# Optimization experiments

Hardware: AMD Instinct MI355X
Metric: run time of the kernel (lower is better)

## Reference

```python
import jax, jax.numpy as jnp
import numpy as np

N = 50000      # num nodes
C_IN = 128     # channels[0]
C_OUT = 128    # channels[1]
D = 16         # fixed node degree
T = 4          # diffusion steps
H_MLP = 64     # diff_mlp hidden
H_GRU = 128    # GRUAggr hidden
EPS = 0.01


def setup_inputs() -> dict:
    key = jax.random.key(0)
    ks = jax.random.split(key, 10)
    node_attr = jax.random.normal(ks[0], (N, C_IN), jnp.float32)
    # adjacency sorted by source: node i owns columns [i*D, i*D+D)
    src = jnp.repeat(jnp.arange(N), D)
    dst = jax.random.randint(ks[1], (N * D,), 0, N)
    edge_index = jnp.stack([src, dst])                       # [2, N*D]
    slices = jnp.stack([jnp.arange(N) * D, jnp.full((N,), D)], axis=1)  # [N,2] (start,count)
    noise = EPS * jax.random.normal(ks[2], (T, N, D), jnp.float32)      # eps*randn per step
    init = lambda k, shape, fan: (jax.random.normal(k, shape, jnp.float32) / np.sqrt(fan))
    W1 = init(ks[3], ((1 + T) * C_IN, H_MLP), (1 + T) * C_IN)
    b1 = jnp.zeros((H_MLP,), jnp.float32)
    W2 = init(ks[4], (H_MLP, 1), H_MLP)
    b2 = jnp.zeros((1,), jnp.float32)
    Wx = init(ks[5], (C_IN, 3 * H_GRU), C_IN)
    Wh = init(ks[6], (H_GRU, 3 * H_GRU), H_GRU)
    bx = jnp.zeros((3 * H_GRU,), jnp.float32)
    bh = jnp.zeros((3 * H_GRU,), jnp.float32)
    Wo = init(ks[7], (H_GRU, C_OUT), H_GRU)
    bo = jnp.zeros((C_OUT,), jnp.float32)
    return dict(node_attr=node_attr, edge_index=edge_index, slices=slices, noise=noise,
                W1=W1, b1=b1, W2=W2, b2=b2, Wx=Wx, Wh=Wh, bx=bx, bh=bh, Wo=Wo, bo=bo)


def _gru(x_seq, Wx, Wh, bx, bh):
    # x_seq: [T+1, N, C]; torch GRU gate order (r, z, n)
    H = Wh.shape[0]
    def step(h, x):
        gx = x @ Wx + bx
        gh = h @ Wh + bh
        xr, xz, xn = jnp.split(gx, 3, axis=-1)
        hr, hz, hn = jnp.split(gh, 3, axis=-1)
        r = jax.nn.sigmoid(xr + hr)
        z = jax.nn.sigmoid(xz + hz)
        n = jnp.tanh(xn + r * hn)
        return (1.0 - z) * n + z * h, None
    h0 = jnp.zeros((x_seq.shape[1], H), x_seq.dtype)
    h, _ = jax.lax.scan(step, h0, x_seq)
    return h


def reference(node_attr, edge_index, slices, noise, W1, b1, W2, b2, Wx, Wh, bx, bh, Wo, bo):
    n, C = node_attr.shape
    t_steps, _, deg = noise.shape
    dst = edge_index[1]
    walk_embeds = jnp.zeros((n, 1 + t_steps, C), node_attr.dtype).at[:, 0, :].set(node_attr)
    cur = jnp.arange(n)
    for t in range(t_steps):
        starts = slices[cur, 0]                              # slice_cat(adj, adj_slic_t)
        nbr = dst[starts[:, None] + jnp.arange(deg)]         # [N, D] neighbor node ids
        v_t = node_attr[nbr]                                 # [N, D, C]
        # diff_mlp on [prefix walk embed | candidate neighbor]: split the first
        # linear layer so the shared prefix is computed once per node (position
        # 1+t of walk_embeds is still zero, matching the original fill order).
        h_pre = walk_embeds.reshape(n, (1 + t_steps) * C) @ W1 + b1       # [N, H_MLP]
        h_nbr = jnp.einsum('ndc,ch->ndh', v_t, W1[(1 + t) * C:(2 + t) * C])
        logp = (jax.nn.relu(h_pre[:, None, :] + h_nbr) @ W2)[..., 0] + b2[0]  # [N, D]
        logp = jax.lax.stop_gradient(logp)                   # torch.no_grad()
        # scatter_logsumexp over init node == logsumexp over the D candidates
        p = jnp.exp(logp - jax.nn.logsumexp(logp, axis=1, keepdims=True)) + noise[t]
        sel = jnp.argmax(p, axis=1)                          # scatter_max per init node
        cur = nbr[jnp.arange(n), sel]                        # walks_t
        walk_embeds = walk_embeds.at[:, 1 + t, :].set(node_attr[cur])
    h = _gru(jnp.transpose(walk_embeds, (1, 0, 2)), Wx, Wh, bx, bh)
    return h @ Wo + bo                                       # [N, C_OUT]
```

## Files before the change

### kernel.cpp

```cpp
#include <hip/hip_runtime.h>
#include <math.h>

#define NND 50000
#define DEG 16

typedef __attribute__((ext_vector_type(8))) short short8v;
typedef __attribute__((ext_vector_type(4))) float float4v;

#define OFF_HPRE 0ULL
#define OFF_PROJ 12800000ULL
#define OFF_XB   64000000ULL
#define OFF_IDX  102400000ULL
#define OFF_BQF  103600384ULL
#define OFF_WOF  103862528ULL
#define WS_NEED  103895296ULL

#define LOG2E 1.44269504088896f

__device__ __forceinline__ float fast_sig(float x){
    return __builtin_amdgcn_rcpf(1.f + __builtin_amdgcn_exp2f(-LOG2E*x));
}
__device__ __forceinline__ float fast_tanh(float x){
    return fmaf(-2.f, __builtin_amdgcn_rcpf(1.f + __builtin_amdgcn_exp2f((2.f*LOG2E)*x)), 1.f);
}
__device__ __forceinline__ unsigned short f2bf(float f){
    unsigned int u = __float_as_uint(f);
    u += 0x7FFFu + ((u >> 16) & 1u);
    return (unsigned short)(u >> 16);
}
__device__ __forceinline__ float bf2f(unsigned short h){
    return __uint_as_float(((unsigned int)h) << 16);
}

__global__ __launch_bounds__(256) void k_iota(int* __restrict__ idx0){
    int i = blockIdx.x*256 + threadIdx.x;
    if (i < NND) idx0[i] = i;
}

__global__ __launch_bounds__(256) void k_projall(const float* __restrict__ A,
    const float* __restrict__ W1, const float* __restrict__ b1,
    float* __restrict__ hpre, float* __restrict__ proj)
{
    __shared__ float Alt[32][320];
    __shared__ float Bl[32][68];
    const int tid = threadIdx.x;
    const int row0 = blockIdx.x << 8;
    const int y = blockIdx.y;
    const float* B = W1 + (size_t)y*128*64;
    const int row_t = tid >> 4, col_t = tid & 15;
    float4 acc[16];
#pragma unroll
    for (int i=0;i<16;i++) acc[i] = make_float4(0.f,0.f,0.f,0.f);

    for (int k0 = 0; k0 < 128; k0 += 32){
        {
            int gr = row0 + tid; if (gr >= NND) gr = NND-1;
            const float* ap = A + (size_t)gr*128 + k0;
            const int sr = tid + ((tid>>4)<<2);
#pragma unroll
            for (int u=0;u<8;u++){
                float4 v = *(const float4*)(ap + (u<<2));
                Alt[(u<<2)+0][sr] = v.x; Alt[(u<<2)+1][sr] = v.y;
                Alt[(u<<2)+2][sr] = v.z; Alt[(u<<2)+3][sr] = v.w;
            }
        }
#pragma unroll
        for (int r=0;r<2;r++){
            int p = (r<<8) + tid;
            int bk = p >> 4, bc = (p & 15) << 2;
            *(float4*)(&Bl[bk][bc]) = *(const float4*)(B + (size_t)(k0+bk)*64 + bc);
        }
        __syncthreads();
#pragma unroll 2
        for (int k=0;k<32;k++){
            const float* ar = &Alt[k][row_t*20];
            float4 a0 = *(const float4*)(ar);
            float4 a1 = *(const float4*)(ar+4);
            float4 a2 = *(const float4*)(ar+8);
            float4 a3 = *(const float4*)(ar+12);
            float4 b  = *(const float4*)(&Bl[k][col_t<<2]);
            float aa[16] = {a0.x,a0.y,a0.z,a0.w, a1.x,a1.y,a1.z,a1.w,
                            a2.x,a2.y,a2.z,a2.w, a3.x,a3.y,a3.z,a3.w};
#pragma unroll
            for (int j=0;j<16;j++){
                acc[j].x = fmaf(aa[j], b.x, acc[j].x);
                acc[j].y = fmaf(aa[j], b.y, acc[j].y);
                acc[j].z = fmaf(aa[j], b.z, acc[j].z);
                acc[j].w = fmaf(aa[j], b.w, acc[j].w);
            }
        }
        __syncthreads();
    }
    float4 bb = make_float4(0.f,0.f,0.f,0.f);
    if (y == 0) bb = *(const float4*)(b1 + (col_t<<2));
    float* dstp = (y == 0) ? hpre : (proj + (size_t)(y-1)*NND*64);
#pragma unroll
    for (int j=0;j<16;j++){
        int gr = row0 + (row_t<<4) + j;
        if (gr < NND){
            float4 o = make_float4(acc[j].x+bb.x, acc[j].y+bb.y, acc[j].z+bb.z, acc[j].w+bb.w);
            *(float4*)(dstp + ((size_t)gr<<6) + (col_t<<2)) = o;
        }
    }
}

__global__ __launch_bounds__(256) void k_walk4(
    const float* __restrict__ hpre0, const float* __restrict__ proj,
    const int* __restrict__ dst, const float* __restrict__ W2,
    const float* __restrict__ b2, const float* __restrict__ noise,
    int* __restrict__ idxb)
{
    const int tid = threadIdx.x;
    const int sg = tid >> 4, l = tid & 15;
    const int gi = (blockIdx.x << 4) + sg;
    float4 hp = *(const float4*)(hpre0 + ((size_t)gi<<6) + (l<<2));
    float4 w2 = *(const float4*)(W2 + (l<<2));
    const float b2s = b2[0];
    int curv = gi;
#pragma unroll 1
    for (int t=0; t<4; t++){
        const float* pj = proj + (size_t)t*NND*64;
        const int nbr = dst[curv*DEG + l];
        float4 val[16];
#pragma unroll
        for (int d=0; d<16; d++){
            int nd = __shfl(nbr, d, 16);
            val[d] = *(const float4*)(pj + ((size_t)nd<<6) + (l<<2));
        }
        float lp = 0.f;
#pragma unroll
        for (int d=0; d<16; d++){
            float4 v = val[d];
            float q =  fmaxf(hp.x+v.x,0.f)*w2.x;
            q = fmaf(fmaxf(hp.y+v.y,0.f), w2.y, q);
            q = fmaf(fmaxf(hp.z+v.z,0.f), w2.z, q);
            q = fmaf(fmaxf(hp.w+v.w,0.f), w2.w, q);
            q += __shfl_xor(q, 1, 16);
            q += __shfl_xor(q, 2, 16);
            q += __shfl_xor(q, 4, 16);
            q += __shfl_xor(q, 8, 16);
            if (l == d) lp = q + b2s;
        }
        float mx = lp;
#pragma unroll
        for (int off=8; off; off>>=1) mx = fmaxf(mx, __shfl_xor(mx, off, 16));
        float s = expf(lp - mx);
#pragma unroll
        for (int off=8; off; off>>=1) s += __shfl_xor(s, off, 16);
        float p = expf(lp - mx - logf(s)) + noise[(size_t)t*NND*DEG + ((size_t)gi<<4) + l];
        float bv = p; int bi = l;
#pragma unroll
        for (int off=8; off; off>>=1){
            float ov = __shfl_xor(bv, off, 16);
            int   oi = __shfl_xor(bi, off, 16);
            if (ov > bv || (ov == bv && oi < bi)){ bv = ov; bi = oi; }
        }
        int sel = __shfl(nbr, bi, 16);
        if (l == 0) idxb[(size_t)(t+1)*NND + gi] = sel;
        float4 u = *(const float4*)(pj + ((size_t)sel<<6) + (l<<2));
        hp.x += u.x; hp.y += u.y; hp.z += u.z; hp.w += u.w;
        curv = sel;
    }
}

__global__ __launch_bounds__(256) void k_pack_x(const float* __restrict__ na,
    unsigned short* __restrict__ Xb)
{
    int i = blockIdx.x*256 + threadIdx.x;
    if (i < NND*32){
        float4 v = *(const float4*)(na + (size_t)i*4);
        unsigned long long pk = (unsigned long long)f2bf(v.x)
            | ((unsigned long long)f2bf(v.y) << 16)
            | ((unsigned long long)f2bf(v.z) << 32)
            | ((unsigned long long)f2bf(v.w) << 48);
        *(unsigned long long*)(Xb + (size_t)i*4) = pk;
    }
}

__global__ __launch_bounds__(256) void k_pack_bqf(const float* __restrict__ Wx,
    const float* __restrict__ Wh, unsigned short* __restrict__ BqF)
{
    int i = blockIdx.x*256 + threadIdx.x;
    int jj = i & 7, lane = (i>>3)&63, ct = (i>>9)&7, c = (i>>12)&7, y = i>>15;
    int g = ct>>1, jh = ct&1, mm = lane&15, quad = lane>>4;
    int jg = (y<<5) + (jh<<4) + mm;
    int k = (c<<5) + (quad<<3) + jj;
    float v = 0.f;
    if (k < 128){
        if (g < 3) v = Wh[k*384 + g*128 + jg];
    } else {
        int kk = k - 128;
        if (g == 0)      v = Wx[kk*384 + jg];
        else if (g == 1) v = Wx[kk*384 + 128 + jg];
        else if (g == 3) v = Wx[kk*384 + 256 + jg];
    }
    BqF[i] = f2bf(v);
}

__global__ __launch_bounds__(256) void k_pack_wof(const float* __restrict__ Wo,
    unsigned short* __restrict__ WoF)
{
    int i = blockIdx.x*256 + threadIdx.x;
    int jj = i & 7, lane = (i>>3)&63, ct = (i>>9)&7, c = i>>12;
    int n = (ct<<4) + (lane&15);
    int k = (c<<5) + ((lane>>4)<<3) + jj;
    WoF[i] = f2bf(Wo[k*128 + n]);
}

__global__ __launch_bounds__(256,2) void k_gru5(
    const unsigned short* __restrict__ Xb,
    const unsigned short* __restrict__ BqF,
    const unsigned short* __restrict__ WoF,
    const float* __restrict__ bx, const float* __restrict__ bh,
    const float* __restrict__ bo, const int* __restrict__ idxb,
    float* __restrict__ out)
{
    __shared__ unsigned short A_l[8192];
    __shared__ unsigned short X_l[16384];
    const int tid = threadIdx.x;
    const int w = tid >> 6, lane = tid & 63;
    const int m = lane & 15, quad = lane >> 4;
    const int row0 = blockIdx.x << 6;
    const int r = tid & 63, q = tid >> 6;
    int gr = row0 + r; if (gr >= NND) gr = NND-1;
    const int rt_s = r >> 4, m_s = r & 15;
    float brr[2], bzz[2], bxn[2], bhn[2];
#pragma unroll
    for (int jh=0; jh<2; jh++){
        int j = (w<<5) + (jh<<4) + m;
        brr[jh] = bx[j] + bh[j];
        bzz[jh] = bx[128+j] + bh[128+j];
        bxn[jh] = bx[256+j];
        bhn[jh] = bh[256+j];
    }
    unsigned short holdv[2][4][4];
    short8v xv[4];
    {
        const int xr = idxb[gr];
        const unsigned short* xrow = Xb + (size_t)xr*128 + (q<<5);
#pragma unroll
        for (int u=0;u<4;u++) xv[u] = *(const short8v*)(xrow + (u<<3));
#pragma unroll
        for (int u=0;u<4;u++)
            *(short8v*)(X_l + (((rt_s<<2)+q)*64 + (u<<4) + m_s)*8) = xv[u];
        const int xr1 = idxb[NND + gr];
        const unsigned short* xrow1 = Xb + (size_t)xr1*128 + (q<<5);
#pragma unroll
        for (int u=0;u<4;u++) xv[u] = *(const short8v*)(xrow1 + (u<<3));
    }
    __syncthreads();

#pragma unroll 1
    for (int s=0; s<5; s++){
        const unsigned short* Xcur = X_l + ((s&1)<<13);
        float4v zero = {0.f,0.f,0.f,0.f};
        float4v acc[32];
#pragma unroll
        for (int i=0;i<32;i++) acc[i] = zero;
        if (s > 0){
#pragma unroll 1
            for (int c=0;c<4;c++){
                short8v afr[4];
#pragma unroll
                for (int rt=0;rt<4;rt++)
                    afr[rt] = *(const short8v*)(A_l + (((rt<<2) + c)*64 + lane)*8);
                const unsigned short* bp = BqF + ((((size_t)w*8 + c)*8)*64 + lane)*8;
#pragma unroll
                for (int ct=0;ct<6;ct++){
                    short8v bf = *(const short8v*)(bp + (ct<<9));
#pragma unroll
                    for (int rt=0;rt<4;rt++)
                        acc[(ct<<2)+rt] = __builtin_amdgcn_mfma_f32_16x16x32_bf16(afr[rt], bf, acc[(ct<<2)+rt], 0,0,0);
                }
            }
        }
#pragma unroll 1
        for (int c=4;c<8;c++){
            short8v afr[4];
#pragma unroll
            for (int rt=0;rt<4;rt++)
                afr[rt] = *(const short8v*)(Xcur + (((rt<<2) + (c&3))*64 + lane)*8);
            const unsigned short* bp = BqF + ((((size_t)w*8 + c)*8)*64 + lane)*8;
#pragma unroll
            for (int cti=0;cti<6;cti++){
                const int ct = (cti < 4) ? cti : (cti + 2);
                short8v bf = *(const short8v*)(bp + (ct<<9));
#pragma unroll
                for (int rt=0;rt<4;rt++)
                    acc[(ct<<2)+rt] = __builtin_amdgcn_mfma_f32_16x16x32_bf16(afr[rt], bf, acc[(ct<<2)+rt], 0,0,0);
            }
        }
        if (s < 4){
            unsigned short* Xnxt = X_l + (((s+1)&1)<<13);
#pragma unroll
            for (int u=0;u<4;u++)
                *(short8v*)(Xnxt + (((rt_s<<2)+q)*64 + (u<<4) + m_s)*8) = xv[u];
            if (s < 3){
                const int xr = idxb[(size_t)(s+2)*NND + gr];
                const unsigned short* xrow = Xb + (size_t)xr*128 + (q<<5);
#pragma unroll
                for (int u=0;u<4;u++) xv[u] = *(const short8v*)(xrow + (u<<3));
            }
        }
#pragma unroll
        for (int jh=0; jh<2; jh++){
#pragma unroll
            for (int rt=0; rt<4; rt++){
#pragma unroll
                for (int r4=0; r4<4; r4++){
                    float rg = fast_sig(acc[(jh<<2)+rt][r4] + brr[jh]);
                    float zg = fast_sig(acc[((2+jh)<<2)+rt][r4] + bzz[jh]);
                    float ng = fast_tanh(acc[((6+jh)<<2)+rt][r4] + bxn[jh] + rg*(acc[((4+jh)<<2)+rt][r4] + bhn[jh]));
                    float hold = (s == 0) ? 0.f : bf2f(holdv[jh][rt][r4]);
                    holdv[jh][rt][r4] = f2bf((1.f - zg)*ng + zg*hold);
                }
            }
        }
        __syncthreads();
#pragma unroll
        for (int jh=0; jh<2; jh++)
#pragma unroll
            for (int rt=0; rt<4; rt++)
#pragma unroll
                for (int r4=0; r4<4; r4++){
                    int ha = ((((rt<<2)+w)*64 + (((jh<<1)+(m>>3))<<4) + (quad<<2)+r4)<<3) + (m&7);
                    A_l[ha] = holdv[jh][rt][r4];
                }
        __syncthreads();
    }
    float4v zero = {0.f,0.f,0.f,0.f};
    float4v acco[8];
#pragma unroll
    for (int i=0;i<8;i++) acco[i] = zero;
    for (int c=0;c<4;c++){
        short8v afr[4];
#pragma unroll
        for (int rt=0;rt<4;rt++)
            afr[rt] = *(const short8v*)(A_l + (((rt<<2) + c)*64 + lane)*8);
#pragma unroll
        for (int cto=0;cto<2;cto++){
            short8v bf = *(const short8v*)(WoF + (((size_t)(c*8 + (w<<1)+cto))*64 + lane)*8);
#pragma unroll
            for (int rt=0;rt<4;rt++)
                acco[(cto<<2)+rt] = __builtin_amdgcn_mfma_f32_16x16x32_bf16(afr[rt], bf, acco[(cto<<2)+rt], 0,0,0);
        }
    }
#pragma unroll
    for (int cto=0; cto<2; cto++){
        int col = (w<<5) + (cto<<4) + m;
        float bb = bo[col];
#pragma unroll
        for (int rt=0; rt<4; rt++){
#pragma unroll
            for (int r4=0; r4<4; r4++){
                int row = row0 + (rt<<4) + (quad<<2) + r4;
                if (row < NND) out[(size_t)row*128 + col] = acco[(cto<<2)+rt][r4] + bb;
            }
        }
    }
}

extern "C" void kernel_launch(void* const* d_in, const int* in_sizes, int n_in,
                              void* d_out, int out_size, void* d_ws, size_t ws_size,
                              hipStream_t stream)
{
    const float* node_attr = (const float*)d_in[0];
    const int*   edge_index= (const int*)  d_in[1];
    const float* noise = (const float*)d_in[3];
    const float* W1 = (const float*)d_in[4];
    const float* b1 = (const float*)d_in[5];
    const float* W2 = (const float*)d_in[6];
    const float* b2 = (const float*)d_in[7];
    const float* Wx = (const float*)d_in[8];
    const float* Wh = (const float*)d_in[9];
    const float* bx = (const float*)d_in[10];
    const float* bh = (const float*)d_in[11];
    const float* Wo = (const float*)d_in[12];
    const float* bo = (const float*)d_in[13];
    const int* dst = edge_index + (size_t)NND*DEG;
    float* out = (float*)d_out;
    if (ws_size < WS_NEED) return;

    char* ws = (char*)d_ws;
    float* hpre = (float*)(ws + OFF_HPRE);
    float* proj = (float*)(ws + OFF_PROJ);
    unsigned short* Xb  = (unsigned short*)(ws + OFF_XB);
    int* idxb = (int*)(ws + OFF_IDX);
    unsigned short* BqF = (unsigned short*)(ws + OFF_BQF);
    unsigned short* WoF = (unsigned short*)(ws + OFF_WOF);

    k_iota<<<dim3(196), dim3(256), 0, stream>>>(idxb);
    k_pack_x  <<<dim3(6250), dim3(256), 0, stream>>>(node_attr, Xb);
    k_pack_bqf<<<dim3(512),  dim3(256), 0, stream>>>(Wx, Wh, BqF);
    k_pack_wof<<<dim3(64),   dim3(256), 0, stream>>>(Wo, WoF);

    k_projall<<<dim3(196, 5), dim3(256), 0, stream>>>(node_attr, W1, b1, hpre, proj);
    k_walk4<<<dim3(3125), dim3(256), 0, stream>>>(hpre, proj, dst, W2, b2, noise, idxb);

    k_gru5<<<dim3(782), dim3(256), 0, stream>>>(Xb, BqF, WoF, bx, bh, bo, idxb, out);
}
```

Baseline: 358.4 us.

## Fuse setup kernels, prefetch GEMM tiles into registers, reuse gathered neighbor projections

The four small pack/iota kernels are merged into one setup launch, which saves launch overhead. The projection GEMM now loads the next K-chunk of A and B into registers while the current chunk is being computed, so global loads overlap with the FMA loop. In the walk kernel, the chosen neighbor's projection is taken from the already-loaded per-candidate values (val[]) instead of being re-gathered from global memory. The tradeoff is higher register pressure in the GEMM and a 16-way select in the walk.

```diff
diff --git a/kernel.cpp b/kernel.cpp
--- a/kernel.cpp
+++ b/kernel.cpp
@@ -32,9 +32,50 @@
     return __uint_as_float(((unsigned int)h) << 16);
 }
 
-__global__ __launch_bounds__(256) void k_iota(int* __restrict__ idx0){
-    int i = blockIdx.x*256 + threadIdx.x;
-    if (i < NND) idx0[i] = i;
+__global__ __launch_bounds__(256) void k_setup(const float* __restrict__ na,
+    const float* __restrict__ Wx, const float* __restrict__ Wh,
+    const float* __restrict__ Wo, unsigned short* __restrict__ Xb,
+    unsigned short* __restrict__ BqF, unsigned short* __restrict__ WoF,
+    int* __restrict__ idx0)
+{
+    const int b = blockIdx.x, tid = threadIdx.x;
+    {
+        int i = b*256 + tid;
+        if (i < NND*32){
+            float4 v = *(const float4*)(na + (size_t)i*4);
+            unsigned long long pk = (unsigned long long)f2bf(v.x)
+                | ((unsigned long long)f2bf(v.y) << 16)
+                | ((unsigned long long)f2bf(v.z) << 32)
+                | ((unsigned long long)f2bf(v.w) << 48);
+            *(unsigned long long*)(Xb + (size_t)i*4) = pk;
+        }
+    }
+    if (b < 512){
+        int i = b*256 + tid;
+        int jj = i & 7, lane = (i>>3)&63, ct = (i>>9)&7, c = (i>>12)&7, y = i>>15;
+        int g = ct>>1, jh = ct&1, mm = lane&15, quad = lane>>4;
+        int jg = (y<<5) + (jh<<4) + mm;
+        int k = (c<<5) + (quad<<3) + jj;
+        float v = 0.f;
+        if (k < 128){
+            if (g < 3) v = Wh[k*384 + g*128 + jg];
+        } else {
+            int kk = k - 128;
+            if (g == 0)      v = Wx[kk*384 + jg];
+            else if (g == 1) v = Wx[kk*384 + 128 + jg];
+            else if (g == 3) v = Wx[kk*384 + 256 + jg];
+        }
+        BqF[i] = f2bf(v);
+    } else if (b < 576){
+        int i = (b-512)*256 + tid;
+        int jj = i & 7, lane = (i>>3)&63, ct = (i>>9)&7, c = i>>12;
+        int n = (ct<<4) + (lane&15);
+        int k = (c<<5) + ((lane>>4)<<3) + jj;
+        WoF[i] = f2bf(Wo[k*128 + n]);
+    } else if (b < 772){
+        int i = (b-576)*256 + tid;
+        if (i < NND) idx0[i] = i;
+    }
 }
 
 __global__ __launch_bounds__(256) void k_projall(const float* __restrict__ A,
@@ -52,25 +93,36 @@
 #pragma unroll
     for (int i=0;i<16;i++) acc[i] = make_float4(0.f,0.f,0.f,0.f);
 
-    for (int k0 = 0; k0 < 128; k0 += 32){
-        {
-            int gr = row0 + tid; if (gr >= NND) gr = NND-1;
-            const float* ap = A + (size_t)gr*128 + k0;
-            const int sr = tid + ((tid>>4)<<2);
-#pragma unroll
-            for (int u=0;u<8;u++){
-                float4 v = *(const float4*)(ap + (u<<2));
-                Alt[(u<<2)+0][sr] = v.x; Alt[(u<<2)+1][sr] = v.y;
-                Alt[(u<<2)+2][sr] = v.z; Alt[(u<<2)+3][sr] = v.w;
-            }
-        }
-#pragma unroll
-        for (int r=0;r<2;r++){
-            int p = (r<<8) + tid;
-            int bk = p >> 4, bc = (p & 15) << 2;
-            *(float4*)(&Bl[bk][bc]) = *(const float4*)(B + (size_t)(k0+bk)*64 + bc);
-        }
+    int gr = row0 + tid; if (gr >= NND) gr = NND-1;
+    const float* ap = A + (size_t)gr*128;
+    const int sr = tid + ((tid>>4)<<2);
+    const int bk = tid >> 4, bc = (tid & 15) << 2;
+    const int bk1 = (256+tid) >> 4, bc1 = (tid & 15) << 2;
+
+    float4 pa[8];
+    float4 pb0, pb1;
+#pragma unroll
+    for (int u=0;u<8;u++) pa[u] = *(const float4*)(ap + (u<<2));
+    pb0 = *(const float4*)(B + (size_t)bk*64 + bc);
+    pb1 = *(const float4*)(B + (size_t)bk1*64 + bc1);
+
+#pragma unroll 1
+    for (int c=0;c<4;c++){
+#pragma unroll
+        for (int u=0;u<8;u++){
+            Alt[(u<<2)+0][sr] = pa[u].x; Alt[(u<<2)+1][sr] = pa[u].y;
+            Alt[(u<<2)+2][sr] = pa[u].z; Alt[(u<<2)+3][sr] = pa[u].w;
+        }
+        *(float4*)(&Bl[bk][bc])   = pb0;
+        *(float4*)(&Bl[bk1][bc1]) = pb1;
         __syncthreads();
+        if (c < 3){
+            const float* apn = ap + ((c+1)<<5);
+#pragma unroll
+            for (int u=0;u<8;u++) pa[u] = *(const float4*)(apn + (u<<2));
+            pb0 = *(const float4*)(B + (size_t)(((c+1)<<5)+bk)*64 + bc);
+            pb1 = *(const float4*)(B + (size_t)(((c+1)<<5)+bk1)*64 + bc1);
+        }
 #pragma unroll 2
         for (int k=0;k<32;k++){
             const float* ar = &Alt[k][row_t*20];
@@ -96,10 +148,10 @@
     float* dstp = (y == 0) ? hpre : (proj + (size_t)(y-1)*NND*64);
 #pragma unroll
     for (int j=0;j<16;j++){
-        int gr = row0 + (row_t<<4) + j;
-        if (gr < NND){
+        int grr = row0 + (row_t<<4) + j;
+        if (grr < NND){
             float4 o = make_float4(acc[j].x+bb.x, acc[j].y+bb.y, acc[j].z+bb.z, acc[j].w+bb.w);
-            *(float4*)(dstp + ((size_t)gr<<6) + (col_t<<2)) = o;
+            *(float4*)(dstp + ((size_t)grr<<6) + (col_t<<2)) = o;
         }
     }
 }
@@ -157,54 +209,14 @@
         }
         int sel = __shfl(nbr, bi, 16);
         if (l == 0) idxb[(size_t)(t+1)*NND + gi] = sel;
-        float4 u = *(const float4*)(pj + ((size_t)sel<<6) + (l<<2));
+        float4 u = val[0];
+#pragma unroll
+        for (int d=1; d<16; d++){
+            if (bi == d) u = val[d];
+        }
         hp.x += u.x; hp.y += u.y; hp.z += u.z; hp.w += u.w;
         curv = sel;
     }
-}
-
-__global__ __launch_bounds__(256) void k_pack_x(const float* __restrict__ na,
-    unsigned short* __restrict__ Xb)
-{
-    int i = blockIdx.x*256 + threadIdx.x;
-    if (i < NND*32){
-        float4 v = *(const float4*)(na + (size_t)i*4);
-        unsigned long long pk = (unsigned long long)f2bf(v.x)
-            | ((unsigned long long)f2bf(v.y) << 16)
-            | ((unsigned long long)f2bf(v.z) << 32)
-            | ((unsigned long long)f2bf(v.w) << 48);
-        *(unsigned long long*)(Xb + (size_t)i*4) = pk;
-    }
-}
-
-__global__ __launch_bounds__(256) void k_pack_bqf(const float* __restrict__ Wx,
-    const float* __restrict__ Wh, unsigned short* __restrict__ BqF)
-{
-    int i = blockIdx.x*256 + threadIdx.x;
-    int jj = i & 7, lane = (i>>3)&63, ct = (i>>9)&7, c = (i>>12)&7, y = i>>15;
-    int g = ct>>1, jh = ct&1, mm = lane&15, quad = lane>>4;
-    int jg = (y<<5) + (jh<<4) + mm;
-    int k = (c<<5) + (quad<<3) + jj;
-    float v = 0.f;
-    if (k < 128){
-        if (g < 3) v = Wh[k*384 + g*128 + jg];
-    } else {
-        int kk = k - 128;
-        if (g == 0)      v = Wx[kk*384 + jg];
-        else if (g == 1) v = Wx[kk*384 + 128 + jg];
-        else if (g == 3) v = Wx[kk*384 + 256 + jg];
-    }
-    BqF[i] = f2bf(v);
-}
-
-__global__ __launch_bounds__(256) void k_pack_wof(const float* __restrict__ Wo,
-    unsigned short* __restrict__ WoF)
-{
-    int i = blockIdx.x*256 + threadIdx.x;
-    int jj = i & 7, lane = (i>>3)&63, ct = (i>>9)&7, c = i>>12;
-    int n = (ct<<4) + (lane&15);
-    int k = (c<<5) + ((lane>>4)<<3) + jj;
-    WoF[i] = f2bf(Wo[k*128 + n]);
 }
 
 __global__ __launch_bounds__(256,2) void k_gru5(
@@ -389,10 +401,7 @@
     unsigned short* BqF = (unsigned short*)(ws + OFF_BQF);
     unsigned short* WoF = (unsigned short*)(ws + OFF_WOF);
 
-    k_iota<<<dim3(196), dim3(256), 0, stream>>>(idxb);
-    k_pack_x  <<<dim3(6250), dim3(256), 0, stream>>>(node_attr, Xb);
-    k_pack_bqf<<<dim3(512),  dim3(256), 0, stream>>>(Wx, Wh, BqF);
-    k_pack_wof<<<dim3(64),   dim3(256), 0, stream>>>(Wo, WoF);
+    k_setup<<<dim3(6250), dim3(256), 0, stream>>>(node_attr, Wx, Wh, Wo, Xb, BqF, WoF, idxb);
 
     k_projall<<<dim3(196, 5), dim3(256), 0, stream>>>(node_attr, W1, b1, hpre, proj);
     k_walk4<<<dim3(3125), dim3(256), 0, stream>>>(hpre, proj, dst, W2, b2, noise, idxb);
```

After: 399.4 us. 1.11x slower.
